# Kernel optimization log

Hardware: AMD Instinct MI355X
Metric: run time of the kernel (lower is better)

Reference implementation:

```python
import jax, jax.numpy as jnp
import numpy as np
import math

HEAD = 4
B, N, C = 8, 1024, 256


def setup_inputs() -> dict:
    key = jax.random.key(0)
    k1, k2, k3, k4, k5 = jax.random.split(key, 5)
    query = jax.random.normal(k1, (B, N, C), dtype=jnp.float32)
    keyt = jax.random.normal(k2, (B, N, C), dtype=jnp.float32)
    value = jax.random.normal(k3, (B, N, C), dtype=jnp.float32)
    mask = jax.random.randint(k4, (B, N, N), 0, 2).astype(bool)
    dis = jax.random.normal(k5, (B, N, N), dtype=jnp.float32)
    return {"query": query, "key": keyt, "value": value, "mask": mask, "dis": dis}


def reference(query, key, value, mask, dis):
    Bq, Nq, Cq = key.shape
    d = Cq // HEAD
    # split heads: [B,N,C] -> [h,B,N,d]
    q = query.reshape(Bq, Nq, HEAD, d).transpose(2, 0, 1, 3)
    k = key.reshape(Bq, Nq, HEAD, d).transpose(2, 0, 1, 3)
    v = value.reshape(Bq, Nq, HEAD, d).transpose(2, 0, 1, 3)
    # scores: [h,B,N,N]; note: dis added BEFORE scaling, as in the torch code
    scores = jnp.einsum('hbnd,hbmd->hbnm', q, k)
    scores = scores + dis[None]            # dis broadcasts over head dim
    scores = scores / math.sqrt(d)
    scores = jnp.where(mask[None], -jnp.inf, scores)
    p_attn = jax.nn.softmax(scores, axis=-1)
    out = jnp.einsum('hbnm,hbmd->hbnd', p_attn, v)  # [h,B,N,d]
    out = out.transpose(1, 2, 0, 3).reshape(Bq, Nq, Cq)
    return out, p_attn
```

## Files before the change

kernel.cpp:

```cpp
#include <hip/hip_runtime.h>
#include <math.h>

#define HEADS 4
#define BATCH 8
#define SEQ   1024
#define CH    256
#define DH    64
#define RB    16
#define NTHR  512
#define SSTR  1032

typedef float  floatx4  __attribute__((ext_vector_type(4)));
typedef float  floatx2  __attribute__((ext_vector_type(2)));
typedef short  shortx8  __attribute__((ext_vector_type(8)));

__device__ __forceinline__ unsigned short f2bf(float f) {
    unsigned u = __float_as_uint(f);
    unsigned r = u + 0x7FFFu + ((u >> 16) & 1u);
    return (unsigned short)(r >> 16);
}
__device__ __forceinline__ float bf2f(unsigned short h) {
    return __uint_as_float(((unsigned)h) << 16);
}
__device__ __forceinline__ shortx8 pack8(float4 a, float4 b) {
    shortx8 r;
    r[0] = (short)f2bf(a.x); r[1] = (short)f2bf(a.y);
    r[2] = (short)f2bf(a.z); r[3] = (short)f2bf(a.w);
    r[4] = (short)f2bf(b.x); r[5] = (short)f2bf(b.y);
    r[6] = (short)f2bf(b.z); r[7] = (short)f2bf(b.w);
    return r;
}

__global__ __launch_bounds__(256)
void prep(const float* __restrict__ q, const float* __restrict__ k,
          const float* __restrict__ v, const void* __restrict__ maskp,
          unsigned short* __restrict__ qb, unsigned short* __restrict__ kb,
          unsigned short* __restrict__ vt, unsigned* __restrict__ pm)
{
    __shared__ unsigned short tl[64][68];
    const int t = threadIdx.x;
    const int bid = blockIdx.x;
    if (bid < 2048) {
        const float* src = (bid < 1024) ? q : k;
        unsigned short* dst = (bid < 1024) ? qb : kb;
        size_t idx = (size_t)(bid & 1023) * 2048 + (size_t)t * 8;
        float4 a = *(const float4*)(src + idx);
        float4 b = *(const float4*)(src + idx + 4);
        *(shortx8*)(dst + idx) = pack8(a, b);
        return;
    }
    if (bid < 2560) {
        const int vb = bid - 2048;
        const int nt = vb & 15, h = (vb >> 4) & 3, b = vb >> 6;
        const int n0 = nt * 64;
        const float* vsrc = v + ((size_t)(b * SEQ + n0)) * CH + h * DH;
        #pragma unroll
        for (int it = 0; it < 4; ++it) {
            int fid = it * 256 + t;
            int n = fid >> 4, cc = (fid & 15) * 4;
            float4 x = *(const float4*)(vsrc + (size_t)n * CH + cc);
            tl[n][cc]     = f2bf(x.x);
            tl[n][cc + 1] = f2bf(x.y);
            tl[n][cc + 2] = f2bf(x.z);
            tl[n][cc + 3] = f2bf(x.w);
        }
        __syncthreads();
        unsigned short* vout = vt + ((size_t)((b * HEADS + h) * DH)) * SEQ + n0;
        #pragma unroll
        for (int it = 0; it < 2; ++it) {
            int cid = it * 256 + t;
            int d = cid >> 3, nc = cid & 7;
            shortx8 r;
            #pragma unroll
            for (int j = 0; j < 8; ++j) r[j] = (short)tl[nc * 8 + j][d];
            *(shortx8*)(vout + (size_t)d * SEQ + nc * 8) = r;
        }
        return;
    }
    const int vb2 = bid - 2560;
    const int b = vb2 >> 7, row8 = vb2 & 127;
    const int sub = t >> 7, c0 = t & 127;
    const int row4 = row8 * 2 + sub;
    int fl;
    {
        const unsigned* mw = (const unsigned*)maskp;
        const int lane = t & 63;
        int found = 0;
        #pragma unroll
        for (int j = 0; j < 16; ++j)
            if (mw[lane * 16 + j] & 0xFFFFFF00u) found = 1;
        fl = (__ballot(found != 0) != 0ULL) ? 1 : 0;
    }
    const unsigned char* m8  = (const unsigned char*)maskp;
    const int*           m32 = (const int*)maskp;
    unsigned u = 0;
    #pragma unroll
    for (int r = 0; r < 4; ++r) {
        #pragma unroll
        for (int mc = 0; mc < 8; ++mc) {
            size_t idx = ((size_t)(b * SEQ + row4 * 4 + r)) * SEQ + mc * 128 + c0;
            int mk = fl ? (int)m8[idx] : m32[idx];
            u |= (mk ? 1u : 0u) << (r * 8 + mc);
        }
    }
    pm[((b * 256 + row4) * 128) + c0] = u;
}

__global__ __launch_bounds__(NTHR)
void attn_mfma(const unsigned short* __restrict__ qb,
               const unsigned short* __restrict__ kbf,
               const unsigned short* __restrict__ vt,
               const unsigned* __restrict__ pm,
               const float* __restrict__ dis, float* __restrict__ out,
               float* __restrict__ pout)
{
    __shared__ unsigned short Sraw[RB][SSTR];
    __shared__ float Opart[RB][65];
    __shared__ float invs[RB];

    const int t   = threadIdx.x;
    const int bid = blockIdx.x;
    const int b   = bid & (BATCH - 1);
    const int h   = (bid >> 3) & (HEADS - 1);
    const int n0  = (bid >> 5) * RB;

    const int lane = t & 63;
    const int w    = t >> 6;
    const int ln   = lane & 15;
    const int qd   = lane >> 4;

    const unsigned mb = pm[((b * 256 + (n0 >> 2) + qd) * 128) + w * 16 + ln];

    const unsigned short* qrow = qb + ((size_t)(b * SEQ + n0 + ln)) * CH + h * DH;
    shortx8 aq0 = *(const shortx8*)(qrow + qd * 8);
    shortx8 aq1 = *(const shortx8*)(qrow + 32 + qd * 8);

    const unsigned short* kbase = kbf + ((size_t)(b * SEQ)) * CH + h * DH;
    const unsigned short* vbase = vt + ((size_t)((b * HEADS + h) * DH)) * SEQ;
    const size_t dib0 = ((size_t)(b * SEQ + n0 + qd * 4)) * SEQ + w * 16 + ln;

    #pragma unroll 4
    for (int mc = 0; mc < 8; ++mc) {
        const int mg = mc * 128 + w * 16 + ln;
        const unsigned short* krow = kbase + (size_t)mg * CH;
        shortx8 b0 = *(const shortx8*)(krow + qd * 8);
        shortx8 b1 = *(const shortx8*)(krow + 32 + qd * 8);
        float dv0 = dis[dib0 + mc * 128];
        float dv1 = dis[dib0 + (size_t)1 * SEQ + mc * 128];
        float dv2 = dis[dib0 + (size_t)2 * SEQ + mc * 128];
        float dv3 = dis[dib0 + (size_t)3 * SEQ + mc * 128];
        floatx4 acc = {0.f, 0.f, 0.f, 0.f};
        acc = __builtin_amdgcn_mfma_f32_16x16x32_bf16(aq0, b0, acc, 0, 0, 0);
        acc = __builtin_amdgcn_mfma_f32_16x16x32_bf16(aq1, b1, acc, 0, 0, 0);
        float sc0 = ((mb >> (0 * 8 + mc)) & 1u) ? -INFINITY : (acc[0] + dv0) * 0.125f;
        float sc1 = ((mb >> (1 * 8 + mc)) & 1u) ? -INFINITY : (acc[1] + dv1) * 0.125f;
        float sc2 = ((mb >> (2 * 8 + mc)) & 1u) ? -INFINITY : (acc[2] + dv2) * 0.125f;
        float sc3 = ((mb >> (3 * 8 + mc)) & 1u) ? -INFINITY : (acc[3] + dv3) * 0.125f;
        Sraw[qd * 4 + 0][mg] = f2bf(sc0);
        Sraw[qd * 4 + 1][mg] = f2bf(sc1);
        Sraw[qd * 4 + 2][mg] = f2bf(sc2);
        Sraw[qd * 4 + 3][mg] = f2bf(sc3);
    }
    __syncthreads();

    {
        const int r = t >> 5, l = t & 31;
        float mx = -INFINITY;
        #pragma unroll
        for (int j = 0; j < 4; ++j) {
            shortx8 sv = *(const shortx8*)&Sraw[r][j * 256 + l * 8];
            #pragma unroll
            for (int e = 0; e < 8; ++e) mx = fmaxf(mx, bf2f((unsigned short)sv[e]));
        }
        #pragma unroll
        for (int off = 16; off; off >>= 1) mx = fmaxf(mx, __shfl_xor(mx, off, 32));
        float sum = 0.f;
        #pragma unroll
        for (int j = 0; j < 4; ++j) {
            shortx8 sv = *(const shortx8*)&Sraw[r][j * 256 + l * 8];
            shortx8 ev;
            #pragma unroll
            for (int e = 0; e < 8; ++e) {
                float x = __expf(bf2f((unsigned short)sv[e]) - mx);
                sum += x;
                ev[e] = (short)f2bf(x);
            }
            *(shortx8*)&Sraw[r][j * 256 + l * 8] = ev;
        }
        #pragma unroll
        for (int off = 16; off; off >>= 1) sum += __shfl_xor(sum, off, 32);
        if (l == 0) invs[r] = 1.0f / sum;
    }
    __syncthreads();

    const int hm = w >> 2;
    const int c  = (w & 3) * 16;
    floatx4 accA = {0.f, 0.f, 0.f, 0.f};
    floatx4 accB = {0.f, 0.f, 0.f, 0.f};
    const unsigned short* vcol = vbase + (size_t)(c + ln) * SEQ;
    #pragma unroll 4
    for (int it = 0; it < 16; it += 2) {
        const int kk0 = hm * 512 + (it >> 1) * 64 + qd * 8;
        const int kk1 = kk0 + 32;
        shortx8 af0  = *(const shortx8*)&Sraw[ln][kk0];
        shortx8 bf0  = *(const shortx8*)(vcol + kk0);
        shortx8 af1  = *(const shortx8*)&Sraw[ln][kk1];
        shortx8 bf1  = *(const shortx8*)(vcol + kk1);
        accA = __builtin_amdgcn_mfma_f32_16x16x32_bf16(af0, bf0, accA, 0, 0, 0);
        accB = __builtin_amdgcn_mfma_f32_16x16x32_bf16(af1, bf1, accB, 0, 0, 0);
    }
    floatx4 acco;
    acco[0] = accA[0] + accB[0];
    acco[1] = accA[1] + accB[1];
    acco[2] = accA[2] + accB[2];
    acco[3] = accA[3] + accB[3];

    if (hm == 1) {
        #pragma unroll
        for (int r = 0; r < 4; ++r) Opart[qd * 4 + r][c + ln] = acco[r];
    }
    __syncthreads();

    if (hm == 0) {
        #pragma unroll
        for (int r = 0; r < 4; ++r) {
            int row = qd * 4 + r;
            float ov = (acco[r] + Opart[row][c + ln]) * invs[row];
            out[((size_t)(b * SEQ + n0 + row)) * CH + h * DH + c + ln] = ov;
        }
    }
    {
        float* prow = pout + ((size_t)((h * BATCH + b) * SEQ + n0)) * SEQ;
        #pragma unroll
        for (int i = 0; i < RB; ++i) {
            const float inv = invs[i];
            unsigned pk = *(const unsigned*)&Sraw[i][t * 2];
            floatx2 pv = { bf2f((unsigned short)(pk & 0xFFFFu)) * inv,
                           bf2f((unsigned short)(pk >> 16)) * inv };
            *(floatx2*)(prow + (size_t)i * SEQ + t * 2) = pv;
        }
    }
}

extern "C" void kernel_launch(void* const* d_in, const int* in_sizes, int n_in,
                              void* d_out, int out_size, void* d_ws, size_t ws_size,
                              hipStream_t stream) {
    const float* q    = (const float*)d_in[0];
    const float* k    = (const float*)d_in[1];
    const float* v    = (const float*)d_in[2];
    const void*  mask = d_in[3];
    const float* dis  = (const float*)d_in[4];
    float* out  = (float*)d_out;
    float* pout = out + (size_t)BATCH * SEQ * CH;

    unsigned short* qb  = (unsigned short*)d_ws;
    unsigned short* kbw = qb  + (size_t)BATCH * SEQ * CH;
    unsigned short* vtw = kbw + (size_t)BATCH * SEQ * CH;
    unsigned*       pmw = (unsigned*)(vtw + (size_t)BATCH * SEQ * CH);
    (void)ws_size;

    prep<<<3584, 256, 0, stream>>>(q, k, v, mask, qb, kbw, vtw, pmw);
    attn_mfma<<<HEADS * BATCH * (SEQ / RB), NTHR, 0, stream>>>(
        qb, kbw, vtw, pmw, dis, out, pout);
}
```

Measured before the change: 284.7 us.

## Keep attention scores in registers and fuse softmax with probability output

```diff
diff --git a/kernel.cpp b/kernel.cpp
--- a/kernel.cpp
+++ b/kernel.cpp
@@ -13,6 +13,7 @@
 typedef float  floatx4  __attribute__((ext_vector_type(4)));
 typedef float  floatx2  __attribute__((ext_vector_type(2)));
 typedef short  shortx8  __attribute__((ext_vector_type(8)));
+typedef short  shortx4  __attribute__((ext_vector_type(4)));
 
 __device__ __forceinline__ unsigned short f2bf(float f) {
     unsigned u = __float_as_uint(f);
@@ -78,9 +79,10 @@
         return;
     }
     const int vb2 = bid - 2560;
-    const int b = vb2 >> 7, row8 = vb2 & 127;
-    const int sub = t >> 7, c0 = t & 127;
-    const int row4 = row8 * 2 + sub;
+    const int b = vb2 >> 7, rg = vb2 & 127;
+    const int sub = t >> 5, wq = t & 31;
+    const int row = rg * 8 + sub;
+    const int w_ = wq >> 2, qd_ = wq & 3;
     int fl;
     {
         const unsigned* mw = (const unsigned*)maskp;
@@ -95,15 +97,16 @@
     const int*           m32 = (const int*)maskp;
     unsigned u = 0;
     #pragma unroll
-    for (int r = 0; r < 4; ++r) {
-        #pragma unroll
-        for (int mc = 0; mc < 8; ++mc) {
-            size_t idx = ((size_t)(b * SEQ + row4 * 4 + r)) * SEQ + mc * 128 + c0;
+    for (int mc = 0; mc < 8; ++mc) {
+        #pragma unroll
+        for (int r = 0; r < 4; ++r) {
+            size_t idx = ((size_t)(b * SEQ + row)) * SEQ
+                       + mc * 128 + w_ * 16 + qd_ * 4 + r;
             int mk = fl ? (int)m8[idx] : m32[idx];
-            u |= (mk ? 1u : 0u) << (r * 8 + mc);
-        }
-    }
-    pm[((b * 256 + row4) * 128) + c0] = u;
+            u |= (mk ? 1u : 0u) << (mc * 4 + r);
+        }
+    }
+    pm[(((size_t)b * SEQ + row) << 5) + wq] = u;
 }
 
 __global__ __launch_bounds__(NTHR)
@@ -117,6 +120,8 @@
     __shared__ unsigned short Sraw[RB][SSTR];
     __shared__ float Opart[RB][65];
     __shared__ float invs[RB];
+    __shared__ float wmax[8][16];
+    __shared__ float wsum[8][16];
 
     const int t   = threadIdx.x;
     const int bid = blockIdx.x;
@@ -129,7 +134,7 @@
     const int ln   = lane & 15;
     const int qd   = lane >> 4;
 
-    const unsigned mb = pm[((b * 256 + (n0 >> 2) + qd) * 128) + w * 16 + ln];
+    const unsigned mb = pm[(((size_t)b * SEQ + n0 + ln) << 5) + w * 4 + qd];
 
     const unsigned short* qrow = qb + ((size_t)(b * SEQ + n0 + ln)) * CH + h * DH;
     shortx8 aq0 = *(const shortx8*)(qrow + qd * 8);
@@ -137,59 +142,66 @@
 
     const unsigned short* kbase = kbf + ((size_t)(b * SEQ)) * CH + h * DH;
     const unsigned short* vbase = vt + ((size_t)((b * HEADS + h) * DH)) * SEQ;
-    const size_t dib0 = ((size_t)(b * SEQ + n0 + qd * 4)) * SEQ + w * 16 + ln;
-
-    #pragma unroll 4
+    const float* disrow =
+        dis + ((size_t)(b * SEQ + n0 + ln)) * SEQ + w * 16 + qd * 4;
+
+    float s[32];
+    #pragma unroll
     for (int mc = 0; mc < 8; ++mc) {
-        const int mg = mc * 128 + w * 16 + ln;
-        const unsigned short* krow = kbase + (size_t)mg * CH;
-        shortx8 b0 = *(const shortx8*)(krow + qd * 8);
-        shortx8 b1 = *(const shortx8*)(krow + 32 + qd * 8);
-        float dv0 = dis[dib0 + mc * 128];
-        float dv1 = dis[dib0 + (size_t)1 * SEQ + mc * 128];
-        float dv2 = dis[dib0 + (size_t)2 * SEQ + mc * 128];
-        float dv3 = dis[dib0 + (size_t)3 * SEQ + mc * 128];
+        const int mgb = mc * 128 + w * 16;
+        const unsigned short* krow = kbase + (size_t)(mgb + ln) * CH;
+        shortx8 kf0 = *(const shortx8*)(krow + qd * 8);
+        shortx8 kf1 = *(const shortx8*)(krow + 32 + qd * 8);
+        float4 dv = *(const float4*)(disrow + mc * 128);
         floatx4 acc = {0.f, 0.f, 0.f, 0.f};
-        acc = __builtin_amdgcn_mfma_f32_16x16x32_bf16(aq0, b0, acc, 0, 0, 0);
-        acc = __builtin_amdgcn_mfma_f32_16x16x32_bf16(aq1, b1, acc, 0, 0, 0);
-        float sc0 = ((mb >> (0 * 8 + mc)) & 1u) ? -INFINITY : (acc[0] + dv0) * 0.125f;
-        float sc1 = ((mb >> (1 * 8 + mc)) & 1u) ? -INFINITY : (acc[1] + dv1) * 0.125f;
-        float sc2 = ((mb >> (2 * 8 + mc)) & 1u) ? -INFINITY : (acc[2] + dv2) * 0.125f;
-        float sc3 = ((mb >> (3 * 8 + mc)) & 1u) ? -INFINITY : (acc[3] + dv3) * 0.125f;
-        Sraw[qd * 4 + 0][mg] = f2bf(sc0);
-        Sraw[qd * 4 + 1][mg] = f2bf(sc1);
-        Sraw[qd * 4 + 2][mg] = f2bf(sc2);
-        Sraw[qd * 4 + 3][mg] = f2bf(sc3);
-    }
-    __syncthreads();
-
-    {
-        const int r = t >> 5, l = t & 31;
-        float mx = -INFINITY;
-        #pragma unroll
-        for (int j = 0; j < 4; ++j) {
-            shortx8 sv = *(const shortx8*)&Sraw[r][j * 256 + l * 8];
-            #pragma unroll
-            for (int e = 0; e < 8; ++e) mx = fmaxf(mx, bf2f((unsigned short)sv[e]));
-        }
-        #pragma unroll
-        for (int off = 16; off; off >>= 1) mx = fmaxf(mx, __shfl_xor(mx, off, 32));
-        float sum = 0.f;
-        #pragma unroll
-        for (int j = 0; j < 4; ++j) {
-            shortx8 sv = *(const shortx8*)&Sraw[r][j * 256 + l * 8];
-            shortx8 ev;
-            #pragma unroll
-            for (int e = 0; e < 8; ++e) {
-                float x = __expf(bf2f((unsigned short)sv[e]) - mx);
-                sum += x;
-                ev[e] = (short)f2bf(x);
-            }
-            *(shortx8*)&Sraw[r][j * 256 + l * 8] = ev;
-        }
-        #pragma unroll
-        for (int off = 16; off; off >>= 1) sum += __shfl_xor(sum, off, 32);
-        if (l == 0) invs[r] = 1.0f / sum;
+        acc = __builtin_amdgcn_mfma_f32_16x16x32_bf16(kf0, aq0, acc, 0, 0, 0);
+        acc = __builtin_amdgcn_mfma_f32_16x16x32_bf16(kf1, aq1, acc, 0, 0, 0);
+        s[mc*4+0] = ((mb >> (mc*4+0)) & 1u) ? -INFINITY : (acc[0] + dv.x) * 0.125f;
+        s[mc*4+1] = ((mb >> (mc*4+1)) & 1u) ? -INFINITY : (acc[1] + dv.y) * 0.125f;
+        s[mc*4+2] = ((mb >> (mc*4+2)) & 1u) ? -INFINITY : (acc[2] + dv.z) * 0.125f;
+        s[mc*4+3] = ((mb >> (mc*4+3)) & 1u) ? -INFINITY : (acc[3] + dv.w) * 0.125f;
+    }
+
+    float mx = s[0];
+    #pragma unroll
+    for (int i = 1; i < 32; ++i) mx = fmaxf(mx, s[i]);
+    mx = fmaxf(mx, __shfl_xor(mx, 16));
+    mx = fmaxf(mx, __shfl_xor(mx, 32));
+    if (qd == 0) wmax[w][ln] = mx;
+    __syncthreads();
+    #pragma unroll
+    for (int j = 0; j < 8; ++j) mx = fmaxf(mx, wmax[j][ln]);
+
+    float sum = 0.f;
+    #pragma unroll
+    for (int i = 0; i < 32; ++i) {
+        float x = __expf(s[i] - mx);
+        s[i] = x;
+        sum += x;
+    }
+    sum += __shfl_xor(sum, 16);
+    sum += __shfl_xor(sum, 32);
+    if (qd == 0) wsum[w][ln] = sum;
+    __syncthreads();
+    float tot = 0.f;
+    #pragma unroll
+    for (int j = 0; j < 8; ++j) tot += wsum[j][ln];
+    const float inv = 1.0f / tot;
+    if (w == 0 && qd == 0) invs[ln] = inv;
+
+    float* prow = pout + ((size_t)((h * BATCH + b) * SEQ + n0 + ln)) * SEQ
+                + w * 16 + qd * 4;
+    #pragma unroll
+    for (int mc = 0; mc < 8; ++mc) {
+        shortx4 ev;
+        ev[0] = (short)f2bf(s[mc*4+0]);
+        ev[1] = (short)f2bf(s[mc*4+1]);
+        ev[2] = (short)f2bf(s[mc*4+2]);
+        ev[3] = (short)f2bf(s[mc*4+3]);
+        *(shortx4*)&Sraw[ln][mc * 128 + w * 16 + qd * 4] = ev;
+        float4 pv = { s[mc*4+0] * inv, s[mc*4+1] * inv,
+                      s[mc*4+2] * inv, s[mc*4+3] * inv };
+        *(float4*)(prow + mc * 128) = pv;
     }
     __syncthreads();
 
@@ -220,24 +232,12 @@
         for (int r = 0; r < 4; ++r) Opart[qd * 4 + r][c + ln] = acco[r];
     }
     __syncthreads();
-
     if (hm == 0) {
         #pragma unroll
         for (int r = 0; r < 4; ++r) {
             int row = qd * 4 + r;
             float ov = (acco[r] + Opart[row][c + ln]) * invs[row];
             out[((size_t)(b * SEQ + n0 + row)) * CH + h * DH + c + ln] = ov;
-        }
-    }
-    {
-        float* prow = pout + ((size_t)((h * BATCH + b) * SEQ + n0)) * SEQ;
-        #pragma unroll
-        for (int i = 0; i < RB; ++i) {
-            const float inv = invs[i];
-            unsigned pk = *(const unsigned*)&Sraw[i][t * 2];
-            floatx2 pv = { bf2f((unsigned short)(pk & 0xFFFFu)) * inv,
-                           bf2f((unsigned short)(pk >> 16)) * inv };
-            *(floatx2*)(prow + (size_t)i * SEQ + t * 2) = pv;
         }
     }
 }
```

Result: slower. 297.0 us (+4.3%).
